# Optimization experiments

Measured on AMD Instinct MI355X. Metric: run time of the kernel, lower is better.

Reference implementation:

```python
import jax, jax.numpy as jnp
import numpy as np

A_BITS = 3
W_BITS = 3

def setup_inputs() -> dict:
    key = jax.random.key(0)
    k1, k2 = jax.random.split(key)
    # activations: small nonnegative ints (will be clipped to [0, 2^A_bits-1])
    x = jax.random.randint(k1, (32, 256, 56, 56), 0, 2 ** A_BITS, dtype=jnp.int32)
    # weights: torch.randint(0, 2**W_bits - 1, ...) -> values in [0, 6]
    weight = jax.random.randint(k2, (256, 256, 3, 3), 0, 2 ** W_BITS - 1).astype(jnp.float32)
    return {"x": x, "weight": weight}

def reference(x, weight):
    # quantize: clip activations to [0, 2^A_bits - 1]; truncate weight to int
    xq = jnp.clip(x.astype(jnp.int32), 0, 2 ** A_BITS - 1).astype(jnp.float32)
    wq = weight.astype(jnp.int32).astype(jnp.float32)  # OIHW, nonneg small ints
    # direct conv2d, stride 1, no padding (VALID). Small ints -> exact in fp32.
    out = jax.lax.conv_general_dilated(
        xq, wq,
        window_strides=(1, 1),
        padding="VALID",
        dimension_numbers=("NCHW", "OIHW", "NCHW"),
    )
    return out  # [32, 256, 54, 54]
```

## Files before the change

kernel.cpp:

```cpp
#include <hip/hip_runtime.h>
#include <stdint.h>

typedef int i32x4 __attribute__((ext_vector_type(4)));
typedef float f32x4 __attribute__((ext_vector_type(4)));

#define N_IMG 32
#define C_IN 256
#define H_IN 56
#define W_IN 56
#define K_OUT 256
#define H_OUT 54
#define W_OUT 54
#define HW_OUT 2916
#define M_PIX 93312
#define CHW_OUT 746496

#define BM 192

#define XT_BYTES ((size_t)N_IMG * H_IN * W_IN * C_IN)
#define WT_BYTES ((size_t)9 * K_OUT * C_IN)

#define HALO_ROWS 448
#define B_OFF 57344
#define B_STRIDE 32768

__global__ __launch_bounds__(256) void xform(const int* __restrict__ x,
                                             const float* __restrict__ w,
                                             unsigned char* __restrict__ xt,
                                             unsigned char* __restrict__ wt) {
    const int bid = blockIdx.x;
    if (bid < N_IMG * H_IN) {
        const int n = bid / H_IN;
        const int h = bid % H_IN;
        const int c = threadIdx.x;
        const int* src = x + ((size_t)((n * C_IN + c) * H_IN + h)) * W_IN;
        unsigned char* dst = xt + ((size_t)(n * H_IN + h) * W_IN) * C_IN + c;
        #pragma unroll
        for (int w0 = 0; w0 < W_IN; w0 += 4) {
            int4 v = *(const int4*)(src + w0);
            int a[4] = {v.x, v.y, v.z, v.w};
            #pragma unroll
            for (int j = 0; j < 4; ++j) {
                int q = a[j] < 0 ? 0 : (a[j] > 7 ? 7 : a[j]);
                dst[(size_t)(w0 + j) * C_IN] = (unsigned char)q;
            }
        }
    } else {
        const int k = bid - N_IMG * H_IN;
        const int c = threadIdx.x;
        const float* src = w + ((size_t)k * C_IN + c) * 9;
        #pragma unroll
        for (int rs = 0; rs < 9; ++rs) {
            int iv = (int)src[rs];
            wt[((size_t)rs * K_OUT + k) * C_IN + c] = (unsigned char)iv;
        }
    }
}

__device__ __forceinline__ void gload_lds16(const void* g, void* l) {
    __builtin_amdgcn_global_load_lds(
        (const __attribute__((address_space(1))) uint32_t*)g,
        (__attribute__((address_space(3))) uint32_t*)l,
        16, 0, 0);
}

__device__ __forceinline__ unsigned lds_off(const void* p) {
    return (unsigned)(unsigned long long)(__attribute__((address_space(3))) const char*)p;
}

#define DSREAD(dst, addr) \
    asm volatile("ds_read_b128 %0, %1" : "=v"(dst) : "v"(addr))

__global__ __launch_bounds__(512) void conv_mfma(const unsigned char* __restrict__ xt,
                                                 const unsigned char* __restrict__ wt,
                                                 float* __restrict__ out) {
    __shared__ __align__(16) unsigned char lds[122880];

    const int t512 = threadIdx.x;
    const int l    = t512 & 63;
    const int wid  = t512 >> 6;
    const int wr   = wid >> 2;
    const int wc   = wid & 3;
    const int mb   = blockIdx.x;

    const int srow = t512 >> 3;
    const int cs   = (((t512 & 7) ^ (srow & 7)) << 4);
    const int tb16 = t512 * 16;

    const int m0  = mb * BM;
    const int n0  = m0 / HW_OUT;
    const int rm0 = m0 - n0 * HW_OUT;
    const int oh0 = rm0 / W_OUT;
    const int ow0 = rm0 - oh0 * W_OUT;
    const int pix0 = n0 * (H_IN * W_IN) + oh0 * W_IN + ow0;

    const int lrow = l & 15;
    int drow[6];
    #pragma unroll
    for (int mf = 0; mf < 6; ++mf) {
        const int m   = m0 + wr * 96 + mf * 16 + lrow;
        const int n   = m / HW_OUT;
        const int rem = m - n * HW_OUT;
        const int oh  = rem / W_OUT;
        const int ow  = rem - oh * W_OUT;
        drow[mf] = n * (H_IN * W_IN) + oh * W_IN + ow - pix0;
    }

    const int lk = (l >> 4) << 4;
    const unsigned swzB = (unsigned)((lrow & 7) << 4);
    unsigned brow128[4];
    #pragma unroll
    for (int nf = 0; nf < 4; ++nf) brow128[nf] = (unsigned)((wc * 64 + nf * 16 + lrow) << 7);
    const unsigned colkB[2] = { ((unsigned)lk) ^ swzB, ((unsigned)(64 + lk)) ^ swzB };

    int bbase[4];
    #pragma unroll
    for (int j = 0; j < 4; ++j) bbase[j] = ((j * 64 + srow) << 8) + cs;

    i32x4 acc[6][4];
    #pragma unroll
    for (int i = 0; i < 6; ++i)
        #pragma unroll
        for (int j = 0; j < 4; ++j)
            acc[i][j] = (i32x4){0, 0, 0, 0};

    const char* xb = (const char*)xt;
    const char* wb = (const char*)wt;
    const unsigned ldsb = lds_off(lds);

    #define STAGE_HALO(CH) do {                                             \
        const char* hsrc_ = xb + (size_t)pix0 * 256 + (size_t)(CH) * 128;   \
        _Pragma("unroll")                                                   \
        for (int i_ = 0; i_ < 7; ++i_)                                      \
            gload_lds16(hsrc_ + (size_t)(((i_ * 64 + srow) << 8) + cs),     \
                        lds + i_ * 8192 + tb16);                            \
    } while (0)

    #define STAGE_B(TAP, CH, SEL) do {                                      \
        const char* bsrc_ = wb + (size_t)(TAP) * (K_OUT * C_IN) + (size_t)(CH) * 128; \
        unsigned char* bdst_ = lds + B_OFF + (size_t)(SEL) * B_STRIDE + tb16; \
        gload_lds16(bsrc_ + bbase[0], bdst_);                               \
        gload_lds16(bsrc_ + bbase[1], bdst_ + 8192);                        \
        gload_lds16(bsrc_ + bbase[2], bdst_ + 16384);                       \
        gload_lds16(bsrc_ + bbase[3], bdst_ + 24576);                       \
    } while (0)

    #define KBODY(G, DO_STAGE) do {                                         \
        const int ch_  = ((G) >= 9) ? 1 : 0;                                \
        const int tap_ = (G) - ch_ * 9;                                     \
        const int r_   = (tap_ * 11) >> 5;                                  \
        const int s_   = tap_ - r_ * 3;                                     \
        const int toff_ = r_ * W_IN + s_;                                   \
        const unsigned bB_ = ldsb + B_OFF + ((unsigned)((G) & 1)) * B_STRIDE; \
        i32x4 a0[6], b0[4], a1[6], b1[4];                                   \
        unsigned abase_[6], aswz_[6];                                       \
        _Pragma("unroll")                                                   \
        for (int mf = 0; mf < 6; ++mf) {                                    \
            const int row_ = drow[mf] + toff_;                              \
            abase_[mf] = ldsb + ((unsigned)row_ << 7);                      \
            aswz_[mf]  = ((unsigned)(row_ & 7)) << 4;                       \
            DSREAD(a0[mf], abase_[mf] + (((unsigned)lk) ^ aswz_[mf]));      \
        }                                                                   \
        _Pragma("unroll")                                                   \
        for (int nf = 0; nf < 4; ++nf) DSREAD(b0[nf], bB_ + brow128[nf] + colkB[0]); \
        if (DO_STAGE) {                                                     \
            const int g1_ = (G) + 1;                                        \
            const int c1_ = (g1_ >= 9) ? 1 : 0;                             \
            STAGE_B(g1_ - c1_ * 9, c1_, (g1_ & 1));                         \
        }                                                                   \
        _Pragma("unroll")                                                   \
        for (int mf = 0; mf < 6; ++mf)                                      \
            DSREAD(a1[mf], abase_[mf] + (((unsigned)(64 + lk)) ^ aswz_[mf])); \
        _Pragma("unroll")                                                   \
        for (int nf = 0; nf < 4; ++nf) DSREAD(b1[nf], bB_ + brow128[nf] + colkB[1]); \
        asm volatile("s_waitcnt lgkmcnt(10)" ::: "memory");                 \
        __builtin_amdgcn_sched_barrier(0);                                  \
        __builtin_amdgcn_s_setprio(1);                                      \
        _Pragma("unroll")                                                   \
        for (int mf = 0; mf < 6; ++mf)                                      \
            _Pragma("unroll")                                               \
            for (int nf = 0; nf < 4; ++nf)                                  \
                acc[mf][nf] = __builtin_amdgcn_mfma_i32_16x16x64_i8(        \
                    a0[mf], b0[nf], acc[mf][nf], 0, 0, 0);                  \
        __builtin_amdgcn_s_setprio(0);                                      \
        asm volatile("s_waitcnt lgkmcnt(0)" ::: "memory");                  \
        __builtin_amdgcn_sched_barrier(0);                                  \
        __builtin_amdgcn_s_setprio(1);                                      \
        _Pragma("unroll")                                                   \
        for (int mf = 0; mf < 6; ++mf)                                      \
            _Pragma("unroll")                                               \
            for (int nf = 0; nf < 4; ++nf)                                  \
                acc[mf][nf] = __builtin_amdgcn_mfma_i32_16x16x64_i8(        \
                    a1[mf], b1[nf], acc[mf][nf], 0, 0, 0);                  \
        __builtin_amdgcn_s_setprio(0);                                      \
    } while (0)

    STAGE_HALO(0);
    STAGE_B(0, 0, 0);
    asm volatile("s_waitcnt vmcnt(0)" ::: "memory");
    __builtin_amdgcn_s_barrier();

    for (int g = 0; g < 18; ++g) {
        KBODY(g, (g < 17));
        if (g < 17) {
            asm volatile("s_waitcnt vmcnt(0)" ::: "memory");
            __builtin_amdgcn_s_barrier();
        }
        if (g == 8) {
            STAGE_HALO(1);
            asm volatile("s_waitcnt vmcnt(0)" ::: "memory");
            __builtin_amdgcn_s_barrier();
        }
    }

    const int c16 = l & 15;
    const int p4  = (l >> 4) << 2;
    #pragma unroll
    for (int mf = 0; mf < 6; ++mf) {
        const int m   = mb * BM + wr * 96 + mf * 16 + p4;
        const int n   = m / HW_OUT;
        const int rem = m - n * HW_OUT;
        float* ob = out + (size_t)n * CHW_OUT + rem;
        #pragma unroll
        for (int nf = 0; nf < 4; ++nf) {
            const int ch = wc * 64 + nf * 16 + c16;
            f32x4 v;
            #pragma unroll
            for (int j = 0; j < 4; ++j) v[j] = (float)acc[mf][nf][j];
            *(f32x4*)(ob + (size_t)ch * HW_OUT) = v;
        }
    }
    #undef KBODY
    #undef STAGE_B
    #undef STAGE_HALO
}

__global__ __launch_bounds__(256) void conv_naive(const int* __restrict__ x,
                                                  const float* __restrict__ w,
                                                  float* __restrict__ out) {
    int idx = blockIdx.x * 256 + threadIdx.x;
    if (idx >= N_IMG * K_OUT * HW_OUT) return;
    const int wo = idx % W_OUT;
    int tmp = idx / W_OUT;
    const int ho = tmp % H_OUT; tmp /= H_OUT;
    const int k = tmp % K_OUT;
    const int n = tmp / K_OUT;
    float acc = 0.f;
    for (int c = 0; c < C_IN; ++c) {
        const int* xp = x + ((size_t)((n * C_IN + c) * H_IN + ho)) * W_IN + wo;
        const float* wp = w + ((size_t)(k * C_IN + c)) * 9;
        #pragma unroll
        for (int r = 0; r < 3; ++r)
            #pragma unroll
            for (int s = 0; s < 3; ++s) {
                int xv = xp[r * W_IN + s];
                xv = xv < 0 ? 0 : (xv > 7 ? 7 : xv);
                acc += (float)xv * (float)(int)wp[r * 3 + s];
            }
    }
    out[idx] = acc;
}

extern "C" void kernel_launch(void* const* d_in, const int* in_sizes, int n_in,
                              void* d_out, int out_size, void* d_ws, size_t ws_size,
                              hipStream_t stream) {
    const int*   x = (const int*)d_in[0];
    const float* w = (const float*)d_in[1];
    float* out = (float*)d_out;

    const size_t need = XT_BYTES + WT_BYTES;
    if (ws_size >= need) {
        unsigned char* xt = (unsigned char*)d_ws;
        unsigned char* wt = (unsigned char*)((char*)d_ws + XT_BYTES);
        hipLaunchKernelGGL(xform, dim3(N_IMG * H_IN + K_OUT), dim3(256), 0, stream,
                           x, w, xt, wt);
        hipLaunchKernelGGL(conv_mfma, dim3(M_PIX / BM), dim3(512), 0, stream,
                           xt, wt, out);
    } else {
        const int total = N_IMG * K_OUT * HW_OUT;
        hipLaunchKernelGGL(conv_naive, dim3((total + 255) / 256), dim3(256), 0, stream, x, w, out);
    }
}
```

Before: 94.61 us.

## Load weights directly from global into registers, shrink LDS to halo only

Weights are re-laid out in the transform kernel into an MFMA-fragment-friendly order so each lane can load its B fragments straight from global memory into registers, double-buffered across taps. Shared memory now holds only the activation halo, dropping the per-tap B staging and most of the block barriers. The smaller LDS footprint and a launch_bounds hint aim for two blocks per CU for better latency hiding. The risks are more global/L2 traffic for the weights, since each wave reloads them with no LDS sharing, and higher register pressure from the doubled B buffers under the occupancy target.

```diff
diff --git a/kernel.cpp b/kernel.cpp
--- a/kernel.cpp
+++ b/kernel.cpp
@@ -19,10 +19,6 @@
 
 #define XT_BYTES ((size_t)N_IMG * H_IN * W_IN * C_IN)
 #define WT_BYTES ((size_t)9 * K_OUT * C_IN)
-
-#define HALO_ROWS 448
-#define B_OFF 57344
-#define B_STRIDE 32768
 
 __global__ __launch_bounds__(256) void xform(const int* __restrict__ x,
                                              const float* __restrict__ w,
@@ -46,13 +42,18 @@
             }
         }
     } else {
-        const int k = bid - N_IMG * H_IN;
+        const int o = bid - N_IMG * H_IN;
         const int c = threadIdx.x;
-        const float* src = w + ((size_t)k * C_IN + c) * 9;
+        const float* src = w + ((size_t)o * C_IN + c) * 9;
+        const int h  = c >> 7;
+        const int kk = (c >> 6) & 1;
+        const int g  = (c >> 4) & 3;
+        const int b  = c & 15;
         #pragma unroll
         for (int rs = 0; rs < 9; ++rs) {
             int iv = (int)src[rs];
-            wt[((size_t)rs * K_OUT + k) * C_IN + c] = (unsigned char)iv;
+            wt[(size_t)((rs * 2 + h) * 2 + kk) * 16384 + o * 64 + g * 16 + b]
+                = (unsigned char)iv;
         }
     }
 }
@@ -64,17 +65,10 @@
         16, 0, 0);
 }
 
-__device__ __forceinline__ unsigned lds_off(const void* p) {
-    return (unsigned)(unsigned long long)(__attribute__((address_space(3))) const char*)p;
-}
-
-#define DSREAD(dst, addr) \
-    asm volatile("ds_read_b128 %0, %1" : "=v"(dst) : "v"(addr))
-
-__global__ __launch_bounds__(512) void conv_mfma(const unsigned char* __restrict__ xt,
-                                                 const unsigned char* __restrict__ wt,
-                                                 float* __restrict__ out) {
-    __shared__ __align__(16) unsigned char lds[122880];
+__global__ __launch_bounds__(512, 2) void conv_mfma(const unsigned char* __restrict__ xt,
+                                                    const unsigned char* __restrict__ wt,
+                                                    float* __restrict__ out) {
+    __shared__ __align__(16) unsigned char halo[57344];
 
     const int t512 = threadIdx.x;
     const int l    = t512 & 63;
@@ -83,9 +77,11 @@
     const int wc   = wid & 3;
     const int mb   = blockIdx.x;
 
+    const int slot = t512 & 7;
     const int srow = t512 >> 3;
-    const int cs   = (((t512 & 7) ^ (srow & 7)) << 4);
+    const int cs   = ((slot ^ (srow & 7)) << 4);
     const int tb16 = t512 * 16;
+    const int sb   = srow * 256 + cs;
 
     const int m0  = mb * BM;
     const int n0  = m0 / HW_OUT;
@@ -106,16 +102,13 @@
         drow[mf] = n * (H_IN * W_IN) + oh * W_IN + ow - pix0;
     }
 
-    const int lk = (l >> 4) << 4;
-    const unsigned swzB = (unsigned)((lrow & 7) << 4);
-    unsigned brow128[4];
-    #pragma unroll
-    for (int nf = 0; nf < 4; ++nf) brow128[nf] = (unsigned)((wc * 64 + nf * 16 + lrow) << 7);
-    const unsigned colkB[2] = { ((unsigned)lk) ^ swzB, ((unsigned)(64 + lk)) ^ swzB };
-
-    int bbase[4];
-    #pragma unroll
-    for (int j = 0; j < 4; ++j) bbase[j] = ((j * 64 + srow) << 8) + cs;
+    const unsigned g16 = (unsigned)((l >> 4) << 4);
+
+    const char* wb = (const char*)wt;
+    const char* bptr[4];
+    #pragma unroll
+    for (int nf = 0; nf < 4; ++nf)
+        bptr[nf] = wb + (wc * 64 + nf * 16 + (l & 15)) * 64 + (l >> 4) * 16;
 
     i32x4 acc[6][4];
     #pragma unroll
@@ -125,93 +118,74 @@
             acc[i][j] = (i32x4){0, 0, 0, 0};
 
     const char* xb = (const char*)xt;
-    const char* wb = (const char*)wt;
-    const unsigned ldsb = lds_off(lds);
-
-    #define STAGE_HALO(CH) do {                                             \
-        const char* hsrc_ = xb + (size_t)pix0 * 256 + (size_t)(CH) * 128;   \
-        _Pragma("unroll")                                                   \
-        for (int i_ = 0; i_ < 7; ++i_)                                      \
-            gload_lds16(hsrc_ + (size_t)(((i_ * 64 + srow) << 8) + cs),     \
-                        lds + i_ * 8192 + tb16);                            \
+
+    #define STAGE_HALO(H) do {                                               \
+        const char* hs_ = xb + (size_t)pix0 * 256 + (H) * 128 + sb;          \
+        _Pragma("unroll")                                                    \
+        for (int i_ = 0; i_ < 7; ++i_)                                       \
+            gload_lds16(hs_ + (size_t)i_ * 16384, halo + i_ * 8192 + tb16);  \
     } while (0)
 
-    #define STAGE_B(TAP, CH, SEL) do {                                      \
-        const char* bsrc_ = wb + (size_t)(TAP) * (K_OUT * C_IN) + (size_t)(CH) * 128; \
-        unsigned char* bdst_ = lds + B_OFF + (size_t)(SEL) * B_STRIDE + tb16; \
-        gload_lds16(bsrc_ + bbase[0], bdst_);                               \
-        gload_lds16(bsrc_ + bbase[1], bdst_ + 8192);                        \
-        gload_lds16(bsrc_ + bbase[2], bdst_ + 16384);                       \
-        gload_lds16(bsrc_ + bbase[3], bdst_ + 24576);                       \
+    #define LOADB(B, TAP, H) do {                                            \
+        const int bo_ = ((TAP) * 2 + (H)) * 32768;                           \
+        _Pragma("unroll")                                                    \
+        for (int nf = 0; nf < 4; ++nf) {                                     \
+            B[nf][0] = *(const i32x4*)(bptr[nf] + bo_);                      \
+            B[nf][1] = *(const i32x4*)(bptr[nf] + bo_ + 16384);              \
+        }                                                                    \
     } while (0)
 
-    #define KBODY(G, DO_STAGE) do {                                         \
-        const int ch_  = ((G) >= 9) ? 1 : 0;                                \
-        const int tap_ = (G) - ch_ * 9;                                     \
-        const int r_   = (tap_ * 11) >> 5;                                  \
-        const int s_   = tap_ - r_ * 3;                                     \
-        const int toff_ = r_ * W_IN + s_;                                   \
-        const unsigned bB_ = ldsb + B_OFF + ((unsigned)((G) & 1)) * B_STRIDE; \
-        i32x4 a0[6], b0[4], a1[6], b1[4];                                   \
-        unsigned abase_[6], aswz_[6];                                       \
-        _Pragma("unroll")                                                   \
-        for (int mf = 0; mf < 6; ++mf) {                                    \
-            const int row_ = drow[mf] + toff_;                              \
-            abase_[mf] = ldsb + ((unsigned)row_ << 7);                      \
-            aswz_[mf]  = ((unsigned)(row_ & 7)) << 4;                       \
-            DSREAD(a0[mf], abase_[mf] + (((unsigned)lk) ^ aswz_[mf]));      \
-        }                                                                   \
-        _Pragma("unroll")                                                   \
-        for (int nf = 0; nf < 4; ++nf) DSREAD(b0[nf], bB_ + brow128[nf] + colkB[0]); \
-        if (DO_STAGE) {                                                     \
-            const int g1_ = (G) + 1;                                        \
-            const int c1_ = (g1_ >= 9) ? 1 : 0;                             \
-            STAGE_B(g1_ - c1_ * 9, c1_, (g1_ & 1));                         \
-        }                                                                   \
-        _Pragma("unroll")                                                   \
-        for (int mf = 0; mf < 6; ++mf)                                      \
-            DSREAD(a1[mf], abase_[mf] + (((unsigned)(64 + lk)) ^ aswz_[mf])); \
-        _Pragma("unroll")                                                   \
-        for (int nf = 0; nf < 4; ++nf) DSREAD(b1[nf], bB_ + brow128[nf] + colkB[1]); \
-        asm volatile("s_waitcnt lgkmcnt(10)" ::: "memory");                 \
-        __builtin_amdgcn_sched_barrier(0);                                  \
-        __builtin_amdgcn_s_setprio(1);                                      \
-        _Pragma("unroll")                                                   \
-        for (int mf = 0; mf < 6; ++mf)                                      \
-            _Pragma("unroll")                                               \
-            for (int nf = 0; nf < 4; ++nf)                                  \
-                acc[mf][nf] = __builtin_amdgcn_mfma_i32_16x16x64_i8(        \
-                    a0[mf], b0[nf], acc[mf][nf], 0, 0, 0);                  \
-        __builtin_amdgcn_s_setprio(0);                                      \
-        asm volatile("s_waitcnt lgkmcnt(0)" ::: "memory");                  \
-        __builtin_amdgcn_sched_barrier(0);                                  \
-        __builtin_amdgcn_s_setprio(1);                                      \
-        _Pragma("unroll")                                                   \
-        for (int mf = 0; mf < 6; ++mf)                                      \
-            _Pragma("unroll")                                               \
-            for (int nf = 0; nf < 4; ++nf)                                  \
-                acc[mf][nf] = __builtin_amdgcn_mfma_i32_16x16x64_i8(        \
-                    a1[mf], b1[nf], acc[mf][nf], 0, 0, 0);                  \
-        __builtin_amdgcn_s_setprio(0);                                      \
+    #define TILE(B, TAP) do {                                                \
+        const int toff_ = ((TAP) / 3) * W_IN + ((TAP) % 3);                  \
+        _Pragma("unroll")                                                    \
+        for (int kk = 0; kk < 2; ++kk) {                                     \
+            i32x4 av_[6];                                                    \
+            _Pragma("unroll")                                                \
+            for (int mf = 0; mf < 6; ++mf) {                                 \
+                const int row_ = drow[mf] + toff_;                           \
+                const unsigned off_ = ((unsigned)row_ << 7) +                \
+                    (((unsigned)(kk << 6) + g16) ^ ((unsigned)(row_ & 7) << 4)); \
+                av_[mf] = *(const i32x4*)(halo + off_);                      \
+            }                                                                \
+            _Pragma("unroll")                                                \
+            for (int mf = 0; mf < 6; ++mf)                                   \
+                _Pragma("unroll")                                            \
+                for (int nf = 0; nf < 4; ++nf)                               \
+                    acc[mf][nf] = __builtin_amdgcn_mfma_i32_16x16x64_i8(     \
+                        av_[mf], B[nf][kk], acc[mf][nf], 0, 0, 0);           \
+        }                                                                    \
     } while (0)
 
+    i32x4 b0[4][2], b1[4][2];
+
     STAGE_HALO(0);
-    STAGE_B(0, 0, 0);
+    LOADB(b0, 0, 0);
     asm volatile("s_waitcnt vmcnt(0)" ::: "memory");
     __builtin_amdgcn_s_barrier();
 
-    for (int g = 0; g < 18; ++g) {
-        KBODY(g, (g < 17));
-        if (g < 17) {
-            asm volatile("s_waitcnt vmcnt(0)" ::: "memory");
-            __builtin_amdgcn_s_barrier();
-        }
-        if (g == 8) {
-            STAGE_HALO(1);
-            asm volatile("s_waitcnt vmcnt(0)" ::: "memory");
-            __builtin_amdgcn_s_barrier();
-        }
-    }
+    #pragma unroll
+    for (int t = 0; t < 8; t += 2) {
+        LOADB(b1, t + 1, 0);
+        TILE(b0, t);
+        LOADB(b0, t + 2, 0);
+        TILE(b1, t + 1);
+    }
+    LOADB(b1, 0, 1);
+    TILE(b0, 8);
+
+    __builtin_amdgcn_s_barrier();
+    STAGE_HALO(1);
+    asm volatile("s_waitcnt vmcnt(0)" ::: "memory");
+    __builtin_amdgcn_s_barrier();
+
+    #pragma unroll
+    for (int t = 0; t < 8; t += 2) {
+        LOADB(b0, t + 1, 1);
+        TILE(b1, t);
+        LOADB(b1, t + 2, 1);
+        TILE(b0, t + 1);
+    }
+    TILE(b1, 8);
 
     const int c16 = l & 15;
     const int p4  = (l >> 4) << 2;
@@ -230,8 +204,8 @@
             *(f32x4*)(ob + (size_t)ch * HW_OUT) = v;
         }
     }
-    #undef KBODY
-    #undef STAGE_B
+    #undef TILE
+    #undef LOADB
     #undef STAGE_HALO
 }
 
```

After: 94.72 us. No clear change (+0.1%).
